# Kernel optimization log

Hardware: AMD Instinct MI355X
Metric: run time of the kernel (lower is better)

The kernel has to match this reference:

```python
import jax, jax.numpy as jnp
import numpy as np

BETA = 0.95      # leak
THRESH = 1.0     # snntorch Leaky default threshold
ALPHA = 2.0      # ATan surrogate alpha (atan_with_alpha)
T = 100          # SPIKE_STEPS
D_IN = 65536     # input_dims
HID = 256        # fc1 hidden (hardcoded)
N_OUT = 20       # n_actions(2) * NUM_NEURONS_PER_ACTION(10)


def spike_fn(x):
    # forward of snntorch surrogate.ATan: Heaviside
    return (x > 0.0).astype(x.dtype)


def lif_step(mem, cur):
    # snntorch Leaky, reset_mechanism='subtract':
    # reset computed from previous membrane (detached), then decay+integrate, then fire
    reset = jax.lax.stop_gradient((mem > THRESH).astype(mem.dtype))
    mem_new = BETA * mem + cur - reset * THRESH
    spk = spike_fn(mem_new - THRESH)
    return spk, mem_new


def _run_net(x, W1, b1, W2, b2):
    # x: [T, D_IN]. Precompute all layer-1 currents as one big GEMM, then scan the recurrence.
    cur1_all = x @ W1.T + b1  # [T, HID]

    def step(carry, cur1):
        mem1, mem2 = carry
        spk1, mem1 = lif_step(mem1, cur1)
        cur2 = spk1 @ W2.T + b2  # [n_out]
        spk2, mem2 = lif_step(mem2, cur2)
        return (mem1, mem2), spk2

    init = (jnp.zeros((W1.shape[0],), x.dtype), jnp.zeros((W2.shape[0],), x.dtype))
    (_, mem2_final), spk2_hist = jax.lax.scan(step, init, cur1_all)
    return spk2_hist, mem2_final  # [T, n_out], [n_out]


def setup_inputs() -> dict:
    key = jax.random.key(0)
    ks = jax.random.split(key, 5)
    s = 0.01
    return {
        "poisson_spikes": jax.random.uniform(ks[0], (T, 1, D_IN), dtype=jnp.float32),
        "aW1": jax.random.normal(ks[1], (HID, D_IN), dtype=jnp.float32) * s,
        "ab1": jnp.zeros((HID,), jnp.float32),
        "aW2": jax.random.normal(ks[2], (N_OUT, HID), dtype=jnp.float32) * s,
        "ab2": jnp.zeros((N_OUT,), jnp.float32),
        "cW1": jax.random.normal(ks[3], (HID, D_IN), dtype=jnp.float32) * s,
        "cb1": jnp.zeros((HID,), jnp.float32),
        "cW2": jax.random.normal(ks[4], (1, HID), dtype=jnp.float32) * s,
        "cb2": jnp.zeros((1,), jnp.float32),
    }


def reference(poisson_spikes, aW1, ab1, aW2, ab2, cW1, cb1, cW2, cb2):
    x = poisson_spikes[:, 0, :]  # effective batch of 1 -> [T, D_IN]
    actor_spk_hist, _ = _run_net(x, aW1, ab1, aW2, ab2)        # [T, 20]
    _, critic_mem = _run_net(x, cW1, cb1, cW2, cb2)            # [1]
    spk_sum = actor_spk_hist.sum(axis=0)                       # [20] (sum over timesteps)
    action_vals = jnp.stack([spk_sum[:10].sum(), spk_sum[10:].sum()])
    policy = jax.nn.softmax(action_vals)                       # [2]
    return policy, critic_mem
```

## Files before the change

### kernel.cpp

```cpp
#include <hip/hip_runtime.h>
#include <hip/hip_bf16.h>

#define T_STEPS 100
#define D_IN    65536
#define HID     256
#define HTOT    512
#define BETA    0.95f
#define THRESH  1.0f
#define CHUNK   256
#define ROWS    128

typedef __bf16 bf16x8 __attribute__((ext_vector_type(8)));
typedef float  f32x16 __attribute__((ext_vector_type(16)));

__global__ __launch_bounds__(512) void k_gemm1(
    const float* __restrict__ x,
    const float* __restrict__ aW1,
    const float* __restrict__ cW1,
    float* __restrict__ P,
    int Kc)
{
    const int half = blockIdx.x;
    const int s    = blockIdx.y;
    const int tid  = threadIdx.x;
    const int lane = tid & 63;
    const int l31  = lane & 31;
    const int wv   = tid >> 6;
    const int wt   = (wv & 1) * 64;
    const int hq   = (wv >> 1) * 64;

    __shared__ __bf16 Ah[ROWS][CHUNK];
    __shared__ __bf16 Am[ROWS][CHUNK];

    const float* Wsrc = half ? cW1 : aW1;
    const float* w0 = Wsrc + (size_t)(hq + l31) * D_IN + (lane >> 5) * 8;
    const float* w1 = w0 + (size_t)32 * D_IN;

    const int sr  = tid >> 2;
    const int skq = tid & 3;
    const float* xrow = x + (size_t)sr * D_IN;

    f32x16 acc[2][2];
#pragma unroll
    for (int p = 0; p < 2; p++)
#pragma unroll
        for (int q = 0; q < 2; q++)
#pragma unroll
            for (int i = 0; i < 16; i++) acc[p][q][i] = 0.f;

    const int k0      = s * Kc;
    const int nchunks = Kc / CHUNK;

#define LOADB(d0, d0b, d1, d1b, sn) do {                                      \
    const float* p0_ = w0 + kb + (sn) * 16;                                   \
    const float* p1_ = w1 + kb + (sn) * 16;                                   \
    d0  = *(const float4*)(p0_);                                              \
    d0b = *(const float4*)(p0_ + 4);                                          \
    d1  = *(const float4*)(p1_);                                              \
    d1b = *(const float4*)(p1_ + 4);                                          \
} while (0)

#define STEP(c0, c0b, c1, c1b, sn) do {                                       \
    const int slot_ = (sn) * 2 + (lane >> 5);                                 \
    const int r0_ = wt + l31, r1_ = r0_ + 32;                                 \
    const int pe0_ = ((slot_ ^ (r0_ & 7)) << 3);                              \
    const int pe1_ = ((slot_ ^ (r1_ & 7)) << 3);                              \
    bf16x8 a0h = *(const bf16x8*)&Ah[r0_][pe0_];                              \
    bf16x8 a0m = *(const bf16x8*)&Am[r0_][pe0_];                              \
    bf16x8 a1h = *(const bf16x8*)&Ah[r1_][pe1_];                              \
    bf16x8 a1m = *(const bf16x8*)&Am[r1_][pe1_];                              \
    float f0_[8] = {c0.x, c0.y, c0.z, c0.w, c0b.x, c0b.y, c0b.z, c0b.w};      \
    float f1_[8] = {c1.x, c1.y, c1.z, c1.w, c1b.x, c1b.y, c1b.z, c1b.w};      \
    bf16x8 b0h, b0m, b1h, b1m;                                                \
    _Pragma("unroll")                                                         \
    for (int e = 0; e < 8; e++) {                                             \
        __bf16 h0 = (__bf16)f0_[e];                                           \
        b0h[e] = h0; b0m[e] = (__bf16)(f0_[e] - (float)h0);                   \
        __bf16 h1 = (__bf16)f1_[e];                                           \
        b1h[e] = h1; b1m[e] = (__bf16)(f1_[e] - (float)h1);                   \
    }                                                                         \
    acc[0][0] = __builtin_amdgcn_mfma_f32_32x32x16_bf16(a0m, b0h, acc[0][0], 0,0,0); \
    acc[0][0] = __builtin_amdgcn_mfma_f32_32x32x16_bf16(a0h, b0m, acc[0][0], 0,0,0); \
    acc[0][0] = __builtin_amdgcn_mfma_f32_32x32x16_bf16(a0h, b0h, acc[0][0], 0,0,0); \
    acc[0][1] = __builtin_amdgcn_mfma_f32_32x32x16_bf16(a0m, b1h, acc[0][1], 0,0,0); \
    acc[0][1] = __builtin_amdgcn_mfma_f32_32x32x16_bf16(a0h, b1m, acc[0][1], 0,0,0); \
    acc[0][1] = __builtin_amdgcn_mfma_f32_32x32x16_bf16(a0h, b1h, acc[0][1], 0,0,0); \
    acc[1][0] = __builtin_amdgcn_mfma_f32_32x32x16_bf16(a1m, b0h, acc[1][0], 0,0,0); \
    acc[1][0] = __builtin_amdgcn_mfma_f32_32x32x16_bf16(a1h, b0m, acc[1][0], 0,0,0); \
    acc[1][0] = __builtin_amdgcn_mfma_f32_32x32x16_bf16(a1h, b0h, acc[1][0], 0,0,0); \
    acc[1][1] = __builtin_amdgcn_mfma_f32_32x32x16_bf16(a1m, b1h, acc[1][1], 0,0,0); \
    acc[1][1] = __builtin_amdgcn_mfma_f32_32x32x16_bf16(a1h, b1m, acc[1][1], 0,0,0); \
    acc[1][1] = __builtin_amdgcn_mfma_f32_32x32x16_bf16(a1h, b1h, acc[1][1], 0,0,0); \
} while (0)

    for (int c = 0; c < nchunks; c++) {
        const int kb = k0 + c * CHUNK;
        if (c) __syncthreads();
#pragma unroll
        for (int g = 0; g < 8; g++) {
            const int ko = skq * 64 + g * 8;
            float4 v0 = make_float4(0.f, 0.f, 0.f, 0.f), v1 = v0;
            if (sr < T_STEPS) {
                v0 = *(const float4*)(xrow + kb + ko);
                v1 = *(const float4*)(xrow + kb + ko + 4);
            }
            float f[8] = {v0.x, v0.y, v0.z, v0.w, v1.x, v1.y, v1.z, v1.w};
            bf16x8 hi, mi;
#pragma unroll
            for (int e = 0; e < 8; e++) {
                __bf16 h = (__bf16)f[e];
                hi[e] = h; mi[e] = (__bf16)(f[e] - (float)h);
            }
            const int slot = skq * 8 + g;
            const int pe   = ((slot ^ (sr & 7)) << 3);
            *(bf16x8*)&Ah[sr][pe] = hi;
            *(bf16x8*)&Am[sr][pe] = mi;
        }
        __syncthreads();

        float4 bA0, bA0b, bA1, bA1b, bB0, bB0b, bB1, bB1b;
        LOADB(bA0, bA0b, bA1, bA1b, 0);
#pragma unroll
        for (int s2 = 0; s2 < 8; s2++) {
            const int s0 = 2 * s2, s1 = 2 * s2 + 1;
            LOADB(bB0, bB0b, bB1, bB1b, s1);
            STEP(bA0, bA0b, bA1, bA1b, s0);
            if (s1 < 15) LOADB(bA0, bA0b, bA1, bA1b, s1 + 1);
            STEP(bB0, bB0b, bB1, bB1b, s1);
        }
    }
#undef LOADB
#undef STEP

    const int rbase = 4 * (lane >> 5);
    float* Pb = P + (size_t)s * T_STEPS * HTOT;
#pragma unroll
    for (int p = 0; p < 2; p++)
#pragma unroll
        for (int q = 0; q < 2; q++) {
            const int hcol = half * 256 + hq + q * 32 + l31;
#pragma unroll
            for (int reg = 0; reg < 16; reg++) {
                const int row = (reg & 3) + rbase + 8 * (reg >> 2);
                const int t   = wt + p * 32 + row;
                if (t < T_STEPS) Pb[(size_t)t * HTOT + hcol] = acc[p][q][reg];
            }
        }
}

__global__ __launch_bounds__(256) void k_reduce(
    const float* __restrict__ P,
    const float* __restrict__ ab1, const float* __restrict__ cb1,
    float* __restrict__ cur1, int NS)
{
    int g4 = blockIdx.x * 256 + threadIdx.x;
    int g  = g4 * 4;
    int h0 = g & (HTOT - 1);
    float4 sum;
    sum.x = (h0 + 0 < HID) ? ab1[h0 + 0] : cb1[h0 + 0 - HID];
    sum.y = (h0 + 1 < HID) ? ab1[h0 + 1] : cb1[h0 + 1 - HID];
    sum.z = (h0 + 2 < HID) ? ab1[h0 + 2] : cb1[h0 + 2 - HID];
    sum.w = (h0 + 3 < HID) ? ab1[h0 + 3] : cb1[h0 + 3 - HID];
    for (int ss = 0; ss < NS; ss++) {
        float4 v = *(const float4*)(P + (size_t)ss * T_STEPS * HTOT + g);
        sum.x += v.x; sum.y += v.y; sum.z += v.z; sum.w += v.w;
    }
    *(float4*)(cur1 + g) = sum;
}

__global__ __launch_bounds__(64) void k_lif1(
    const float* __restrict__ cur1,
    unsigned long long* __restrict__ bitsws,
    float* __restrict__ wsa)
{
    const int b    = blockIdx.x;
    const int lane = threadIdx.x;
    const int n    = b * 64 + lane;

    float mem = 0.f;
    for (int tb = 0; tb < T_STEPS; tb += 10) {
        float c[10];
#pragma unroll
        for (int i = 0; i < 10; i++) c[i] = cur1[(size_t)(tb + i) * HTOT + n];
#pragma unroll
        for (int i = 0; i < 10; i++) {
            float reset = (mem > THRESH) ? THRESH : 0.f;
            mem = BETA * mem + c[i] - reset;
            unsigned long long m = __ballot(mem > THRESH);
            if (lane == 0) bitsws[(size_t)(tb + i) * 8 + b] = m;
        }
    }
    if (b == 0 && lane == 0) { wsa[0] = 0.f; wsa[1] = 0.f; }
}

__global__ __launch_bounds__(128) void k_gemm2(
    const unsigned long long* __restrict__ bitsws,
    const float* __restrict__ aW2, const float* __restrict__ ab2,
    const float* __restrict__ cW2, const float* __restrict__ cb2,
    float* __restrict__ wsa, float* __restrict__ out)
{
    const int j   = blockIdx.x;
    const int tid = threadIdx.x;

    __shared__ float W[256];
    __shared__ float c2[T_STEPS];

    const float* Wsrc = (j < 20) ? (aW2 + j * 256) : cW2;
    for (int i = tid; i < 256; i += 128) W[i] = Wsrc[i];
    const float bias  = (j < 20) ? ab2[j] : cb2[0];
    const int   wbase = (j < 20) ? 0 : 4;
    __syncthreads();

    const int t = tid;
    if (t < T_STEPS) {
        unsigned long long m0 = bitsws[(size_t)t * 8 + wbase + 0];
        unsigned long long m1 = bitsws[(size_t)t * 8 + wbase + 1];
        unsigned long long m2 = bitsws[(size_t)t * 8 + wbase + 2];
        unsigned long long m3 = bitsws[(size_t)t * 8 + wbase + 3];
        float acc = bias;
#pragma unroll
        for (int bitp = 0; bitp < 64; bitp++) {
            acc += ((m0 >> bitp) & 1ULL) ? W[bitp]       : 0.f;
            acc += ((m1 >> bitp) & 1ULL) ? W[64 + bitp]  : 0.f;
            acc += ((m2 >> bitp) & 1ULL) ? W[128 + bitp] : 0.f;
            acc += ((m3 >> bitp) & 1ULL) ? W[192 + bitp] : 0.f;
        }
        c2[t] = acc;
    }
    __syncthreads();

    if (tid == 0) {
        float mem = 0.f, spk = 0.f;
        for (int tt = 0; tt < T_STEPS; tt++) {
            float reset = (mem > THRESH) ? THRESH : 0.f;
            mem = BETA * mem + c2[tt] - reset;
            spk += (mem > THRESH) ? 1.f : 0.f;
        }
        if (j < 10)       atomicAdd(&wsa[0], spk);
        else if (j < 20)  atomicAdd(&wsa[1], spk);
        else              out[2] = mem;
    }
}

__global__ __launch_bounds__(64) void k_final(
    const float* __restrict__ wsa, float* __restrict__ out)
{
    if (threadIdx.x == 0) {
        float a0 = wsa[0], a1 = wsa[1];
        float mx = fmaxf(a0, a1);
        float e0 = expf(a0 - mx), e1 = expf(a1 - mx);
        float inv = 1.f / (e0 + e1);
        out[0] = e0 * inv;
        out[1] = e1 * inv;
    }
}

extern "C" void kernel_launch(void* const* d_in, const int* in_sizes, int n_in,
                              void* d_out, int out_size, void* d_ws, size_t ws_size,
                              hipStream_t stream) {
    const float* x   = (const float*)d_in[0];
    const float* aW1 = (const float*)d_in[1];
    const float* ab1 = (const float*)d_in[2];
    const float* aW2 = (const float*)d_in[3];
    const float* ab2 = (const float*)d_in[4];
    const float* cW1 = (const float*)d_in[5];
    const float* cb1 = (const float*)d_in[6];
    const float* cW2 = (const float*)d_in[7];
    const float* cb2 = (const float*)d_in[8];
    float* out = (float*)d_out;

    int NS = 128;
    while (NS > 8 &&
           ((size_t)(NS + 1) * T_STEPS * HTOT) * sizeof(float) + 8192 > ws_size)
        NS >>= 1;
    int Kc = D_IN / NS;

    float* P    = (float*)d_ws;
    float* cur1 = P + (size_t)NS * T_STEPS * HTOT;
    unsigned long long* bitsws =
        (unsigned long long*)(cur1 + T_STEPS * HTOT);
    float* wsa  = (float*)(bitsws + T_STEPS * 8);

    k_gemm1 <<<dim3(2, NS), 512, 0, stream>>>(x, aW1, cW1, P, Kc);
    k_reduce<<<(T_STEPS * HTOT / 4) / 256, 256, 0, stream>>>(P, ab1, cb1, cur1, NS);
    k_lif1  <<<8, 64, 0, stream>>>(cur1, bitsws, wsa);
    k_gemm2 <<<21, 128, 0, stream>>>(bitsws, aW2, ab2, cW2, cb2, wsa, out);
    k_final <<<1, 64, 0, stream>>>(wsa, out);
}
```

Before: 105.3 us.

## Use 1024-thread GEMM1 blocks with one 32-column B tile per wave

Doubles the k_gemm1 block size to 1024 threads, so each of the 16 waves owns a single 32-column slice of W1 instead of two. This halves per-wave accumulators and B-fragment registers and raises the number of waves streaming W1 from global memory at once. The B loads now use a three-deep rotating register buffer with two slices of lookahead. The cost is fewer MFMAs per shared-memory A read, so reuse of the staged x tile per wave drops, and the launch bound of 1024 threads with a minimum-blocks hint could force register limits or spills.

```diff
diff --git a/kernel.cpp b/kernel.cpp
--- a/kernel.cpp
+++ b/kernel.cpp
@@ -13,7 +13,7 @@
 typedef __bf16 bf16x8 __attribute__((ext_vector_type(8)));
 typedef float  f32x16 __attribute__((ext_vector_type(16)));
 
-__global__ __launch_bounds__(512) void k_gemm1(
+__global__ __launch_bounds__(1024, 4) void k_gemm1(
     const float* __restrict__ x,
     const float* __restrict__ aW1,
     const float* __restrict__ cW1,
@@ -27,82 +27,34 @@
     const int l31  = lane & 31;
     const int wv   = tid >> 6;
     const int wt   = (wv & 1) * 64;
-    const int hq   = (wv >> 1) * 64;
+    const int hq   = (wv >> 1) * 32;
 
     __shared__ __bf16 Ah[ROWS][CHUNK];
     __shared__ __bf16 Am[ROWS][CHUNK];
 
     const float* Wsrc = half ? cW1 : aW1;
     const float* w0 = Wsrc + (size_t)(hq + l31) * D_IN + (lane >> 5) * 8;
-    const float* w1 = w0 + (size_t)32 * D_IN;
-
-    const int sr  = tid >> 2;
-    const int skq = tid & 3;
-    const float* xrow = x + (size_t)sr * D_IN;
-
-    f32x16 acc[2][2];
-#pragma unroll
-    for (int p = 0; p < 2; p++)
-#pragma unroll
-        for (int q = 0; q < 2; q++)
-#pragma unroll
-            for (int i = 0; i < 16; i++) acc[p][q][i] = 0.f;
+
+    const int sr = tid >> 3;
+    const float* xrow = x + (size_t)sr * D_IN + (tid & 7) * 8;
+    const bool xok = (sr < T_STEPS);
+
+    f32x16 acc0, acc1;
+#pragma unroll
+    for (int i = 0; i < 16; i++) { acc0[i] = 0.f; acc1[i] = 0.f; }
 
     const int k0      = s * Kc;
     const int nchunks = Kc / CHUNK;
-
-#define LOADB(d0, d0b, d1, d1b, sn) do {                                      \
-    const float* p0_ = w0 + kb + (sn) * 16;                                   \
-    const float* p1_ = w1 + kb + (sn) * 16;                                   \
-    d0  = *(const float4*)(p0_);                                              \
-    d0b = *(const float4*)(p0_ + 4);                                          \
-    d1  = *(const float4*)(p1_);                                              \
-    d1b = *(const float4*)(p1_ + 4);                                          \
-} while (0)
-
-#define STEP(c0, c0b, c1, c1b, sn) do {                                       \
-    const int slot_ = (sn) * 2 + (lane >> 5);                                 \
-    const int r0_ = wt + l31, r1_ = r0_ + 32;                                 \
-    const int pe0_ = ((slot_ ^ (r0_ & 7)) << 3);                              \
-    const int pe1_ = ((slot_ ^ (r1_ & 7)) << 3);                              \
-    bf16x8 a0h = *(const bf16x8*)&Ah[r0_][pe0_];                              \
-    bf16x8 a0m = *(const bf16x8*)&Am[r0_][pe0_];                              \
-    bf16x8 a1h = *(const bf16x8*)&Ah[r1_][pe1_];                              \
-    bf16x8 a1m = *(const bf16x8*)&Am[r1_][pe1_];                              \
-    float f0_[8] = {c0.x, c0.y, c0.z, c0.w, c0b.x, c0b.y, c0b.z, c0b.w};      \
-    float f1_[8] = {c1.x, c1.y, c1.z, c1.w, c1b.x, c1b.y, c1b.z, c1b.w};      \
-    bf16x8 b0h, b0m, b1h, b1m;                                                \
-    _Pragma("unroll")                                                         \
-    for (int e = 0; e < 8; e++) {                                             \
-        __bf16 h0 = (__bf16)f0_[e];                                           \
-        b0h[e] = h0; b0m[e] = (__bf16)(f0_[e] - (float)h0);                   \
-        __bf16 h1 = (__bf16)f1_[e];                                           \
-        b1h[e] = h1; b1m[e] = (__bf16)(f1_[e] - (float)h1);                   \
-    }                                                                         \
-    acc[0][0] = __builtin_amdgcn_mfma_f32_32x32x16_bf16(a0m, b0h, acc[0][0], 0,0,0); \
-    acc[0][0] = __builtin_amdgcn_mfma_f32_32x32x16_bf16(a0h, b0m, acc[0][0], 0,0,0); \
-    acc[0][0] = __builtin_amdgcn_mfma_f32_32x32x16_bf16(a0h, b0h, acc[0][0], 0,0,0); \
-    acc[0][1] = __builtin_amdgcn_mfma_f32_32x32x16_bf16(a0m, b1h, acc[0][1], 0,0,0); \
-    acc[0][1] = __builtin_amdgcn_mfma_f32_32x32x16_bf16(a0h, b1m, acc[0][1], 0,0,0); \
-    acc[0][1] = __builtin_amdgcn_mfma_f32_32x32x16_bf16(a0h, b1h, acc[0][1], 0,0,0); \
-    acc[1][0] = __builtin_amdgcn_mfma_f32_32x32x16_bf16(a1m, b0h, acc[1][0], 0,0,0); \
-    acc[1][0] = __builtin_amdgcn_mfma_f32_32x32x16_bf16(a1h, b0m, acc[1][0], 0,0,0); \
-    acc[1][0] = __builtin_amdgcn_mfma_f32_32x32x16_bf16(a1h, b0h, acc[1][0], 0,0,0); \
-    acc[1][1] = __builtin_amdgcn_mfma_f32_32x32x16_bf16(a1m, b1h, acc[1][1], 0,0,0); \
-    acc[1][1] = __builtin_amdgcn_mfma_f32_32x32x16_bf16(a1h, b1m, acc[1][1], 0,0,0); \
-    acc[1][1] = __builtin_amdgcn_mfma_f32_32x32x16_bf16(a1h, b1h, acc[1][1], 0,0,0); \
-} while (0)
 
     for (int c = 0; c < nchunks; c++) {
         const int kb = k0 + c * CHUNK;
         if (c) __syncthreads();
 #pragma unroll
-        for (int g = 0; g < 8; g++) {
-            const int ko = skq * 64 + g * 8;
+        for (int j = 0; j < 4; j++) {
             float4 v0 = make_float4(0.f, 0.f, 0.f, 0.f), v1 = v0;
-            if (sr < T_STEPS) {
-                v0 = *(const float4*)(xrow + kb + ko);
-                v1 = *(const float4*)(xrow + kb + ko + 4);
+            if (xok) {
+                v0 = *(const float4*)(xrow + kb + j * 64);
+                v1 = *(const float4*)(xrow + kb + j * 64 + 4);
             }
             float f[8] = {v0.x, v0.y, v0.z, v0.w, v1.x, v1.y, v1.z, v1.w};
             bf16x8 hi, mi;
@@ -111,41 +63,62 @@
                 __bf16 h = (__bf16)f[e];
                 hi[e] = h; mi[e] = (__bf16)(f[e] - (float)h);
             }
-            const int slot = skq * 8 + g;
+            const int slot = (tid & 7) + j * 8;
             const int pe   = ((slot ^ (sr & 7)) << 3);
             *(bf16x8*)&Ah[sr][pe] = hi;
             *(bf16x8*)&Am[sr][pe] = mi;
         }
         __syncthreads();
 
-        float4 bA0, bA0b, bA1, bA1b, bB0, bB0b, bB1, bB1b;
-        LOADB(bA0, bA0b, bA1, bA1b, 0);
-#pragma unroll
-        for (int s2 = 0; s2 < 8; s2++) {
-            const int s0 = 2 * s2, s1 = 2 * s2 + 1;
-            LOADB(bB0, bB0b, bB1, bB1b, s1);
-            STEP(bA0, bA0b, bA1, bA1b, s0);
-            if (s1 < 15) LOADB(bA0, bA0b, bA1, bA1b, s1 + 1);
-            STEP(bB0, bB0b, bB1, bB1b, s1);
-        }
-    }
+        float4 bd0[3], bd1[3];
+#define LOADB(i, sn) do {                                                     \
+    const float* p_ = w0 + kb + (sn) * 16;                                    \
+    bd0[i] = *(const float4*)p_;                                              \
+    bd1[i] = *(const float4*)(p_ + 4);                                        \
+} while (0)
+        LOADB(0, 0);
+        LOADB(1, 1);
+#pragma unroll
+        for (int s16 = 0; s16 < 16; s16++) {
+            if (s16 + 2 < 16) LOADB((s16 + 2) % 3, s16 + 2);
+            const int bi = s16 % 3;
+            float f0_[8] = {bd0[bi].x, bd0[bi].y, bd0[bi].z, bd0[bi].w,
+                            bd1[bi].x, bd1[bi].y, bd1[bi].z, bd1[bi].w};
+            bf16x8 bh, bm;
+#pragma unroll
+            for (int e = 0; e < 8; e++) {
+                __bf16 h = (__bf16)f0_[e];
+                bh[e] = h; bm[e] = (__bf16)(f0_[e] - (float)h);
+            }
+            const int slot = s16 * 2 + (lane >> 5);
+            const int r0 = wt + l31, r1 = r0 + 32;
+            const int pe0 = ((slot ^ (r0 & 7)) << 3);
+            const int pe1 = ((slot ^ (r1 & 7)) << 3);
+            bf16x8 a0h = *(const bf16x8*)&Ah[r0][pe0];
+            bf16x8 a0m = *(const bf16x8*)&Am[r0][pe0];
+            bf16x8 a1h = *(const bf16x8*)&Ah[r1][pe1];
+            bf16x8 a1m = *(const bf16x8*)&Am[r1][pe1];
+            acc0 = __builtin_amdgcn_mfma_f32_32x32x16_bf16(a0m, bh, acc0, 0, 0, 0);
+            acc0 = __builtin_amdgcn_mfma_f32_32x32x16_bf16(a0h, bm, acc0, 0, 0, 0);
+            acc0 = __builtin_amdgcn_mfma_f32_32x32x16_bf16(a0h, bh, acc0, 0, 0, 0);
+            acc1 = __builtin_amdgcn_mfma_f32_32x32x16_bf16(a1m, bh, acc1, 0, 0, 0);
+            acc1 = __builtin_amdgcn_mfma_f32_32x32x16_bf16(a1h, bm, acc1, 0, 0, 0);
+            acc1 = __builtin_amdgcn_mfma_f32_32x32x16_bf16(a1h, bh, acc1, 0, 0, 0);
+        }
 #undef LOADB
-#undef STEP
+    }
 
     const int rbase = 4 * (lane >> 5);
+    const int hcol  = half * 256 + hq + l31;
     float* Pb = P + (size_t)s * T_STEPS * HTOT;
 #pragma unroll
-    for (int p = 0; p < 2; p++)
-#pragma unroll
-        for (int q = 0; q < 2; q++) {
-            const int hcol = half * 256 + hq + q * 32 + l31;
-#pragma unroll
-            for (int reg = 0; reg < 16; reg++) {
-                const int row = (reg & 3) + rbase + 8 * (reg >> 2);
-                const int t   = wt + p * 32 + row;
-                if (t < T_STEPS) Pb[(size_t)t * HTOT + hcol] = acc[p][q][reg];
-            }
-        }
+    for (int reg = 0; reg < 16; reg++) {
+        const int row = (reg & 3) + rbase + 8 * (reg >> 2);
+        const int t0  = wt + row;
+        const int t1  = wt + 32 + row;
+        if (t0 < T_STEPS) Pb[(size_t)t0 * HTOT + hcol] = acc0[reg];
+        if (t1 < T_STEPS) Pb[(size_t)t1 * HTOT + hcol] = acc1[reg];
+    }
 }
 
 __global__ __launch_bounds__(256) void k_reduce(
@@ -281,7 +254,7 @@
         (unsigned long long*)(cur1 + T_STEPS * HTOT);
     float* wsa  = (float*)(bitsws + T_STEPS * 8);
 
-    k_gemm1 <<<dim3(2, NS), 512, 0, stream>>>(x, aW1, cW1, P, Kc);
+    k_gemm1 <<<dim3(2, NS), 1024, 0, stream>>>(x, aW1, cW1, P, Kc);
     k_reduce<<<(T_STEPS * HTOT / 4) / 256, 256, 0, stream>>>(P, ab1, cb1, cur1, NS);
     k_lif1  <<<8, 64, 0, stream>>>(cur1, bitsws, wsa);
     k_gemm2 <<<21, 128, 0, stream>>>(bitsws, aW2, ab2, cW2, cb2, wsa, out);
```

Measured after the change: 99.07 us. -5.9%, faster.
